# Kernel optimization log

Measured on AMD Instinct MI355X. Metric: run time of the kernel, lower is better.

Reference implementation:

```python
import jax, jax.numpy as jnp
import numpy as np
from jax import lax

P = 16        # patch_size
F = 4         # fourier_freq
E = 8         # num_experts
G = 8         # groupnorm groups = min(8, out_channel)
CIN = 128
COUT = 128
EPS = 1e-5


def conv2d(x, w):
    # x: [B,C,H,W], w: [O,I,kh,kw], stride 1, SAME padding
    return lax.conv_general_dilated(x, w, (1, 1), 'SAME',
                                    dimension_numbers=('NCHW', 'OIHW', 'NCHW'))


def group_norm(x, g, b):
    B, C, H, W = x.shape
    xg = x.reshape(B, G, C // G, H, W)
    m = xg.mean(axis=(2, 3, 4), keepdims=True)
    v = xg.var(axis=(2, 3, 4), keepdims=True)
    xn = ((xg - m) * lax.rsqrt(v + EPS)).reshape(B, C, H, W)
    return xn * g[None, :, None, None] + b[None, :, None, None]


def silu(x):
    return x * jax.nn.sigmoid(x)


def fourier_feats(Hp, Wp):
    # Fourier positional encoding of patch centers -> [Hp, Wp, 4F] (= gate_channel)
    cy = (jnp.arange(Hp, dtype=jnp.float32) + 0.5) / Hp
    cx = (jnp.arange(Wp, dtype=jnp.float32) + 0.5) / Wp
    freqs = (2.0 ** jnp.arange(F, dtype=jnp.float32)) * jnp.pi
    ay = cy[:, None] * freqs[None, :]            # [Hp, F]
    ax = cx[:, None] * freqs[None, :]            # [Wp, F]
    fy = jnp.concatenate([jnp.sin(ay), jnp.cos(ay)], axis=-1)  # [Hp, 2F]
    fx = jnp.concatenate([jnp.sin(ax), jnp.cos(ax)], axis=-1)  # [Wp, 2F]
    return jnp.concatenate([
        jnp.broadcast_to(fy[:, None, :], (Hp, Wp, 2 * F)),
        jnp.broadcast_to(fx[None, :, :], (Hp, Wp, 2 * F)),
    ], axis=-1)


def setup_inputs() -> dict:
    key = jax.random.key(0)
    ks = jax.random.split(key, 5)
    B, H, W = 8, 128, 128
    x = jax.random.normal(ks[0], (B, CIN, H, W), dtype=jnp.float32)
    expert_w = jax.random.normal(ks[1], (E, COUT, CIN, 3, 3), dtype=jnp.float32) * 0.02
    expert_g = jnp.ones((E, COUT), dtype=jnp.float32)
    expert_b = jnp.zeros((E, COUT), dtype=jnp.float32)
    router_w = jax.random.normal(ks[2], (4 * F, E), dtype=jnp.float32) * 0.1
    router_b = jnp.zeros((E,), dtype=jnp.float32)
    merge_g = jnp.ones((COUT,), dtype=jnp.float32)
    merge_b = jnp.zeros((COUT,), dtype=jnp.float32)
    gamma = jnp.ones((1,), dtype=jnp.float32) * 0.01
    post_w = jax.random.normal(ks[3], (COUT, COUT, 3, 3), dtype=jnp.float32) * 0.02
    post_g = jnp.ones((COUT,), dtype=jnp.float32)
    post_b = jnp.zeros((COUT,), dtype=jnp.float32)
    return {'x': x, 'expert_w': expert_w, 'expert_g': expert_g, 'expert_b': expert_b,
            'router_w': router_w, 'router_b': router_b, 'merge_g': merge_g,
            'merge_b': merge_b, 'gamma': gamma, 'post_w': post_w,
            'post_g': post_g, 'post_b': post_b}


def reference(x, expert_w, expert_g, expert_b, router_w, router_b,
              merge_g, merge_b, gamma, post_w, post_g, post_b):
    B, C, H, W = x.shape
    Hp, Wp = H // P, W // P

    # RouterGate: positional Fourier features -> per-patch expert weights
    feats = fourier_feats(Hp, Wp)                       # [Hp, Wp, 4F]
    logits = feats @ router_w + router_b                # [Hp, Wp, E]
    wts = jax.nn.softmax(logits, axis=-1)               # [Hp, Wp, E]

    # ConvExperts: conv3x3 -> GN -> SiLU + residual, vmapped over experts
    def expert(w, g, b):
        return silu(group_norm(conv2d(x, w), g, b)) + x

    outs = jax.vmap(expert)(expert_w, expert_g, expert_b)  # [E, B, C, H, W]

    # Broadcast patch weights to pixel resolution and merge
    wmap = jnp.repeat(jnp.repeat(wts, P, axis=0), P, axis=1)  # [H, W, E]
    merged = jnp.einsum('ebchw,hwe->bchw', outs, wmap)        # [B, C, H, W]

    # merge GN + SiLU, gamma-scaled residual
    y = x + gamma[0] * silu(group_norm(merged, merge_g, merge_b))

    # post block: conv3x3 (no bias) -> GN -> SiLU
    out = silu(group_norm(conv2d(y, post_w), post_g, post_b))
    return out
```

## Files before the change

### kernel.cpp

```cpp
#include <hip/hip_runtime.h>
#include <hip/hip_bf16.h>


typedef __attribute__((ext_vector_type(8))) short bf16x8;
typedef __attribute__((ext_vector_type(4))) float f32x4;
typedef __attribute__((ext_vector_type(2))) float f32x2;
typedef __attribute__((ext_vector_type(8))) unsigned short u16x8;
typedef __attribute__((ext_vector_type(4))) unsigned short u16x4;
typedef __attribute__((ext_vector_type(2))) unsigned int u32x2;
typedef __attribute__((ext_vector_type(2))) int i32x2;
typedef __attribute__((ext_vector_type(2))) long lx2;

__device__ __forceinline__ float b2f(unsigned short u) {
  unsigned int v = ((unsigned int)u) << 16;
  return __builtin_bit_cast(float, v);
}
__device__ __forceinline__ unsigned short f2b(float f) {
  __hip_bfloat16 h = __float2bfloat16(f);
  return __builtin_bit_cast(unsigned short, h);
}
__device__ __forceinline__ float fsilu(float x) {
  float e = __expf(-x);
  return x * __builtin_amdgcn_rcpf(1.f + e);
}
__device__ __forceinline__ void gll16(const void* g, void* l) {
  __builtin_amdgcn_global_load_lds(
      (const __attribute__((address_space(1))) unsigned int*)g,
      (__attribute__((address_space(3))) unsigned int*)l, 16, 0, 0);
}
__device__ __forceinline__ unsigned char f2fp8(float v) {
  return (unsigned char)(__builtin_amdgcn_cvt_pk_fp8_f32(v, v, 0, false) & 0xff);
}

#define PLANE8 8652800ull

__global__ void k_router(const float* __restrict__ rw, const float* __restrict__ rb,
                         float* __restrict__ wts) {
  int t = threadIdx.x;
  if (t >= 64) return;
  int py = t >> 3, px = t & 7;
  float cy = (py + 0.5f) / 8.f, cx = (px + 0.5f) / 8.f;
  const float PI = 3.14159265358979323846f;
  float f[16];
#pragma unroll
  for (int k = 0; k < 4; ++k) {
    float fr = (float)(1 << k) * PI;
    f[k] = sinf(cy * fr); f[4 + k] = cosf(cy * fr);
    f[8 + k] = sinf(cx * fr); f[12 + k] = cosf(cx * fr);
  }
  float lg[8], mx = -1e30f;
#pragma unroll
  for (int e = 0; e < 8; ++e) {
    float a = rb[e];
#pragma unroll
    for (int k = 0; k < 16; ++k) a += f[k] * rw[k * 8 + e];
    lg[e] = a; mx = fmaxf(mx, a);
  }
  float s = 0.f;
#pragma unroll
  for (int e = 0; e < 8; ++e) { lg[e] = __expf(lg[e] - mx); s += lg[e]; }
  float inv = 1.f / s;
#pragma unroll
  for (int e = 0; e < 8; ++e) wts[t * 8 + e] = lg[e] * inv;
}

__global__ void k_zborder(unsigned short* __restrict__ xpu,
                          unsigned char* __restrict__ xp8) {
  int idx = blockIdx.x * 256 + threadIdx.x;
  if (idx >= 8 * 516) return;
  int b = idx / 516, pxi = idx - b * 516;
  int r, c;
  if (pxi < 130)      { r = 0;   c = pxi; }
  else if (pxi < 260) { r = 129; c = pxi - 130; }
  else if (pxi < 388) { r = pxi - 260 + 1; c = 0; }
  else                { r = pxi - 388 + 1; c = 129; }
  size_t pix = (size_t)(b * 130 + r) * 130 + c;
  unsigned short* p = xpu + pix * 128;
#pragma unroll
  for (int j = 0; j < 16; ++j) *(u16x8*)(p + j * 8) = (u16x8)0;
#pragma unroll
  for (int cc = 0; cc < 2; ++cc) {
    f32x4* q = (f32x4*)(xp8 + cc * PLANE8 + pix * 64);
#pragma unroll
    for (int j = 0; j < 4; ++j) q[j] = (f32x4)0.f;
  }
}

__global__ void k_build_xpad(const float* __restrict__ x, __hip_bfloat16* __restrict__ xp,
                             unsigned char* __restrict__ xp8) {
  int bx = blockIdx.x;
  int wb = bx & 1, cib = (bx >> 1) & 1;
  int h = (bx >> 2) & 127, b = bx >> 9;
  int w0 = wb * 64, ci0 = cib * 64;
  __shared__ float t[64][65];
  int tid = threadIdx.x;
#pragma unroll
  for (int r = 0; r < 16; ++r) {
    int idx = r * 256 + tid;
    int i = idx >> 6, j = idx & 63;
    t[i][j] = x[(((size_t)b * 128 + ci0 + i) * 128 + h) * 128 + w0 + j];
  }
  __syncthreads();
  unsigned short* xpu = (unsigned short*)xp;
#pragma unroll
  for (int r = 0; r < 2; ++r) {
    int s = r * 256 + tid;
    int px = s >> 3, cg = s & 7;
    size_t pixbase = ((size_t)b * 130 + h + 1) * 130 + (w0 + px + 1);
    float v[8];
    u16x8 bv;
#pragma unroll
    for (int k = 0; k < 8; ++k) { v[k] = t[cg * 8 + k][px]; bv[k] = f2b(v[k]); }
    int ci = ci0 + cg * 8;
    *(u16x8*)(xpu + pixbase * 128 + ci) = bv;
    int pl = ci >> 6, cl = ci & 63;
    int kg = (cl >> 3) & 3, c = cl >> 5;
    int pk0 = __builtin_amdgcn_cvt_pk_fp8_f32(v[0], v[1], 0, false);
    pk0 = __builtin_amdgcn_cvt_pk_fp8_f32(v[2], v[3], pk0, true);
    int pk1 = __builtin_amdgcn_cvt_pk_fp8_f32(v[4], v[5], 0, false);
    pk1 = __builtin_amdgcn_cvt_pk_fp8_f32(v[6], v[7], pk1, true);
    i32x2 pk = {pk0, pk1};
    *(i32x2*)(xp8 + (size_t)pl * PLANE8 + pixbase * 64 + kg * 16 + c * 8) = pk;
  }
}

__global__ void k_build_w(const float* __restrict__ src, __hip_bfloat16* __restrict__ dst) {
  int o = blockIdx.x * 256 + threadIdx.x;
  if (o >= 147456) return;
  int cl = o & 31, co = (o >> 5) & 127;
  int r9 = o >> 12;
  int tp = r9 % 9, cc = r9 / 9;
  int ci = cc * 32 + cl;
  ((unsigned short*)dst)[o] = f2b(src[((size_t)co * 128 + ci) * 9 + tp]);
}

__global__ void k_build_w8(const float* __restrict__ src, unsigned char* __restrict__ dst) {
  int o = blockIdx.x * 256 + threadIdx.x;
  if (o >= 1179648) return;
  int e = o / 147456;
  int r = o - e * 147456;
  int cc2 = r / 73728;
  int r2 = r - cc2 * 73728;
  int tp = r2 >> 13;
  int r3 = r2 & 8191;
  int co = r3 >> 6, p = r3 & 63;
  int kg = p >> 4, c = (p >> 3) & 1, j = p & 7;
  int ci = cc2 * 64 + c * 32 + kg * 8 + j;
  dst[o] = f2fp8(src[(((size_t)e * 128 + co) * 128 + ci) * 9 + tp]);
}

template <int G>
__global__ __launch_bounds__(512, 2) void k_conv8(
    const unsigned char* __restrict__ xp8, const unsigned char* __restrict__ wt8,
    unsigned char* __restrict__ out8base, float* __restrict__ partials) {
  __shared__ __align__(16) char smem[90112];
  const int cpx = (G * 512) >> 3;
  const int nid = (blockIdx.x & 7) * cpx + (blockIdx.x >> 3);
  const int eg = nid & (G - 1);
  const int t0 = nid / G;
  const int b = t0 >> 6, rp = t0 & 63, h0 = rp * 2;
  const unsigned char* wt = wt8 + (size_t)eg * 147456;
  unsigned char* out8 = out8base + (size_t)eg * 16777216ull;

  const int tid = threadIdx.x;
  const int lane = tid & 63, wid = tid >> 6;
  const int wm = wid >> 1, wn = wid & 1;
  const int rl = lane & 15, kg = lane >> 4;
  const int rowA = wm >> 1;
  const int colA = (wm & 1) * 64;

  int aoff[3][4], boff[3][4];
#pragma unroll
  for (int mb = 0; mb < 4; ++mb) {
    int col = colA + mb * 16 + rl;
#pragma unroll
    for (int kx = 0; kx < 3; ++kx) {
      int px = col + kx;
      aoff[kx][mb] = (rowA * 160 + px) * 64 + (kg ^ ((px >> 1) & 3)) * 16;
    }
  }
#pragma unroll
  for (int kx = 0; kx < 3; ++kx)
#pragma unroll
    for (int nb = 0; nb < 4; ++nb) {
      int co = wn * 64 + nb * 16 + rl;
      boff[kx][nb] = 20480 + ((kx * 128 + co) * 4 + (kg ^ ((co >> 1) & 3))) * 16;
    }

  int soff[6], loff[6];
  bool isA[6];
#pragma unroll
  for (int it = 0; it < 6; ++it) {
    int s = it * 512 + tid;
    if (s < 1280) {
      int rw = (s >= 640) ? 1 : 0;
      int off = s - rw * 640;
      int px = off >> 2, q = off & 3;
      int qg = q ^ ((px >> 1) & 3);
      isA[it] = true;
      soff[it] = rw * 8320 + px * 64 + qg * 16;
    } else {
      int s2 = s - 1280;
      int tap = s2 >> 9, r3 = s2 & 511;
      int co = r3 >> 2, q = r3 & 3;
      int qg = q ^ ((co >> 1) & 3);
      isA[it] = false;
      soff[it] = tap * 8192 + co * 64 + qg * 16;
    }
    loff[it] = s * 16;
  }

  f32x4 acc[4][4] = {};

#define STG8(bi, u)                                                            \
  {                                                                            \
    const int cc2_ = (u) / 3, ky_ = (u) % 3;                                   \
    char* D = smem + (bi) * 45056;                                             \
    const unsigned char* abase =                                               \
        xp8 + (size_t)cc2_ * PLANE8 + (size_t)(b * 130 + h0 + ky_) * 8320;     \
    const unsigned char* bbase = wt + cc2_ * 73728 + ky_ * 24576;              \
    _Pragma("unroll")                                                          \
    for (int it = 0; it < 5; ++it)                                             \
      gll16((isA[it] ? abase : bbase) + soff[it], D + loff[it]);               \
    if (tid < 256) gll16(bbase + soff[5], D + loff[5]);                        \
  }

  STG8(0, 0);
  for (int u = 0; u < 6; ++u) {
    const int cur = u & 1;
    __syncthreads();
    if (u + 1 < 6) STG8(cur ^ 1, u + 1);
    const char* Al = smem + cur * 45056;
#pragma unroll
    for (int kx = 0; kx < 3; ++kx) {
      lx2 av[4], bv[4];
#pragma unroll
      for (int mb = 0; mb < 4; ++mb) av[mb] = *(const lx2*)(Al + aoff[kx][mb]);
#pragma unroll
      for (int nb = 0; nb < 4; ++nb) bv[nb] = *(const lx2*)(Al + boff[kx][nb]);
#pragma unroll
      for (int c = 0; c < 2; ++c)
#pragma unroll
        for (int mb = 0; mb < 4; ++mb)
#pragma unroll
          for (int nb = 0; nb < 4; ++nb)
            acc[mb][nb] = __builtin_amdgcn_mfma_f32_16x16x32_fp8_fp8(
                bv[nb][c], av[mb][c], acc[mb][nb], 0, 0, 0);
    }
  }
#undef STG8

  float sv[4] = {0, 0, 0, 0}, qv[4] = {0, 0, 0, 0};
#pragma unroll
  for (int mb = 0; mb < 4; ++mb) {
    int px = colA + mb * 16 + rl;
    int h = h0 + rowA, w = px;
    size_t base = (((size_t)b * 128 + h) * 128 + w) * 128;
#pragma unroll
    for (int nb = 0; nb < 4; ++nb) {
      int co0 = wn * 64 + nb * 16 + kg * 4;
      f32x4 v = acc[mb][nb];
#pragma unroll
      for (int j = 0; j < 4; ++j) { sv[nb] += v[j]; qv[nb] += v[j] * v[j]; }
      int pk = __builtin_amdgcn_cvt_pk_fp8_f32(v[0], v[1], 0, false);
      pk = __builtin_amdgcn_cvt_pk_fp8_f32(v[2], v[3], pk, true);
      *(int*)(out8 + base + co0) = pk;
    }
  }
  __syncthreads();
  float* sg = (float*)smem;
  if (tid < 16) sg[tid] = 0.f;
  __syncthreads();
#pragma unroll
  for (int nb = 0; nb < 4; ++nb) {
    float a = sv[nb], q = qv[nb];
#pragma unroll
    for (int o = 32; o > 0; o >>= 1) { a += __shfl_down(a, o); q += __shfl_down(q, o); }
    if (lane == 0) {
      int g = wn * 4 + nb;
      atomicAdd(&sg[g * 2 + 0], a);
      atomicAdd(&sg[g * 2 + 1], q);
    }
  }
  __syncthreads();
  if (tid < 16)
    partials[((size_t)(eg * 8 + b) * 64 + rp) * 16 + tid] = sg[tid];
}

__global__ __launch_bounds__(256, 2) void k_conv(
    const unsigned short* __restrict__ xpu, const unsigned short* __restrict__ wtu,
    unsigned short* __restrict__ outu, float* __restrict__ partials) {
  __shared__ __align__(16) char smem[69632];
  const int bx0 = blockIdx.x;
  const int nid = (bx0 & 7) * 128 + (bx0 >> 3);
  const int b = nid >> 7, h0 = nid & 127;
  const int tid = threadIdx.x;
  const int lane = tid & 63, wid = tid >> 6;
  const int wm = wid >> 1, wn = wid & 1;
  const int rl = lane & 15, kg = lane >> 4;

  int aoff[3][4], boff[3][4];
#pragma unroll
  for (int mb = 0; mb < 4; ++mb) {
    int w = wm * 64 + mb * 16 + rl;
#pragma unroll
    for (int kx = 0; kx < 3; ++kx) {
      int px = w + kx;
      aoff[kx][mb] = (px * 4 + (kg ^ ((px >> 1) & 3))) * 16;
    }
  }
#pragma unroll
  for (int kx = 0; kx < 3; ++kx)
#pragma unroll
    for (int nb = 0; nb < 4; ++nb) {
      int co = wn * 64 + nb * 16 + rl;
      boff[kx][nb] = 10240 + ((kx * 128 + co) * 4 + (kg ^ ((co >> 1) & 3))) * 16;
    }

  int asoff[3], aloff[3];
#pragma unroll
  for (int it = 0; it < 3; ++it) {
    int s = it * 256 + tid;
    int px = s >> 2, q = s & 3;
    int qg = q ^ ((px >> 1) & 3);
    asoff[it] = px * 256 + (q ^ ((px >> 1) & 3)) * 16;
    (void)qg;
    aloff[it] = s * 16;
  }
  int bsoff[6], bloff[6];
#pragma unroll
  for (int jt = 0; jt < 6; ++jt) {
    int s2 = jt * 256 + tid;
    int t3 = s2 >> 9;
    int r3 = s2 & 511;
    int co = r3 >> 2, q = r3 & 3;
    int qg = q ^ ((co >> 1) & 3);
    bsoff[jt] = t3 * 8192 + co * 64 + qg * 16;
    bloff[jt] = 10240 + s2 * 16;
  }

  f32x4 acc[4][4] = {};
  const char* xpb = (const char*)xpu;
  const char* wtb = (const char*)wtu;

#define STAGE(bi, u)                                                          \
  {                                                                           \
    const int cc_ = (u) / 3, ky_ = (u) % 3;                                   \
    char* D = smem + (bi) * 34816;                                            \
    const char* abase = xpb + (size_t)(b * 130 + h0 + ky_) * 33280 + cc_ * 64;\
    const char* bbase = wtb + cc_ * 73728 + ky_ * 24576;                      \
    _Pragma("unroll")                                                         \
    for (int it = 0; it < 2; ++it)                                            \
      gll16(abase + asoff[it], D + aloff[it]);                                \
    if (tid < 128) gll16(abase + asoff[2], D + aloff[2]);                     \
    _Pragma("unroll")                                                         \
    for (int jt = 0; jt < 6; ++jt)                                            \
      gll16(bbase + bsoff[jt], D + bloff[jt]);                                \
  }

  STAGE(0, 0);
  for (int u = 0; u < 12; ++u) {
    const int cur = u & 1;
    __syncthreads();
    if (u + 1 < 12) STAGE(cur ^ 1, u + 1);
    char* Al = smem + cur * 34816;
#pragma unroll
    for (int kx = 0; kx < 3; ++kx) {
      bf16x8 aF[4], bF[4];
#pragma unroll
      for (int mb = 0; mb < 4; ++mb) aF[mb] = *(const bf16x8*)(Al + aoff[kx][mb]);
#pragma unroll
      for (int nb = 0; nb < 4; ++nb) bF[nb] = *(const bf16x8*)(Al + boff[kx][nb]);
#pragma unroll
      for (int mb = 0; mb < 4; ++mb)
#pragma unroll
        for (int nb = 0; nb < 4; ++nb)
          acc[mb][nb] = __builtin_amdgcn_mfma_f32_16x16x32_bf16(
              bF[nb], aF[mb], acc[mb][nb], 0, 0, 0);
    }
  }
#undef STAGE

  float sv[4] = {0, 0, 0, 0}, qv[4] = {0, 0, 0, 0};
#pragma unroll
  for (int mb = 0; mb < 4; ++mb) {
    int w = wm * 64 + mb * 16 + rl;
    size_t base = (((size_t)b * 128 + h0) * 128 + w) * 128;
#pragma unroll
    for (int nb = 0; nb < 4; ++nb) {
      int co0 = wn * 64 + nb * 16 + kg * 4;
      u16x4 pk;
#pragma unroll
      for (int j = 0; j < 4; ++j) {
        float v = acc[mb][nb][j];
        pk[j] = f2b(v);
        sv[nb] += v; qv[nb] += v * v;
      }
      *(u16x4*)(outu + base + co0) = pk;
    }
  }
  __syncthreads();
  float* sg = (float*)smem;
  if (tid < 16) sg[tid] = 0.f;
  __syncthreads();
#pragma unroll
  for (int nb = 0; nb < 4; ++nb) {
    float a = sv[nb], q = qv[nb];
#pragma unroll
    for (int o = 32; o > 0; o >>= 1) { a += __shfl_down(a, o); q += __shfl_down(q, o); }
    if (lane == 0) {
      int g = wn * 4 + nb;
      atomicAdd(&sg[g * 2 + 0], a);
      atomicAdd(&sg[g * 2 + 1], q);
    }
  }
  __syncthreads();
  if (tid < 16) partials[(size_t)nid * 16 + tid] = sg[tid];
}

__global__ void k_redstats(const float* __restrict__ partials, float* __restrict__ stats,
                           int nper) {
  int set = blockIdx.x;
  const float* p = partials + (size_t)set * 8 * nper * 16;
  float* st = stats + set * 128;
  int t = threadIdx.x;
  int o = t >> 2, j = t & 3;
  int b = o >> 4, slot = o & 15;
  int chunk = nper >> 2;
  float s = 0.f;
  for (int i = j * chunk; i < (j + 1) * chunk; ++i)
    s += p[((size_t)b * nper + i) * 16 + slot];
  s += __shfl_xor(s, 1);
  s += __shfl_xor(s, 2);
  if (j == 0) st[o] = s;
}

__global__ void k_redstats2(const float* __restrict__ p2, float* __restrict__ st) {
  int o = blockIdx.x;
  int b = o >> 4, slot = o & 15;
  float s = 0.f;
  for (int i = threadIdx.x; i < 1024; i += 256)
    s += p2[((size_t)b * 1024 + i) * 16 + slot];
#pragma unroll
  for (int off = 32; off > 0; off >>= 1) s += __shfl_down(s, off);
  __shared__ float wsm[4];
  int lane = threadIdx.x & 63, wv = threadIdx.x >> 6;
  if (lane == 0) wsm[wv] = s;
  __syncthreads();
  if (threadIdx.x == 0) st[o] = wsm[0] + wsm[1] + wsm[2] + wsm[3];
}

template <int NEXP>
__global__ void k_merge(const unsigned char* __restrict__ c0,
                        const unsigned char* __restrict__ c1,
                        const unsigned char* __restrict__ c2,
                        const unsigned char* __restrict__ c3,
                        const float* __restrict__ st, const float* __restrict__ eg,
                        const float* __restrict__ eb, const float* __restrict__ wts,
                        unsigned short* __restrict__ merged,
                        const unsigned short* __restrict__ xp,
                        float* __restrict__ partials2, int e0, int flags) {
  __shared__ float sg[16];
  int tid = threadIdx.x;
  if (tid < 16) sg[tid] = 0.f;
  __syncthreads();
  size_t idx = ((size_t)blockIdx.x * 256 + tid) * 8;
  int co0 = (int)(idx & 127);
  size_t pix = idx >> 7;
  int w = (int)(pix & 127), h = (int)((pix >> 7) & 127), b = (int)(pix >> 14);
  int g = co0 >> 4;
  const float cnt = 16.f * 128.f * 128.f;
  int patch = (h >> 4) * 8 + (w >> 4);
  const unsigned char* cs[4] = {c0, c1, c2, c3};
  float a[8] = {0, 0, 0, 0, 0, 0, 0, 0};
#pragma unroll
  for (int k = 0; k < NEXP; ++k) {
    int e = e0 + k;
    float mean = st[e * 128 + (b * 8 + g) * 2] / cnt;
    float var = st[e * 128 + (b * 8 + g) * 2 + 1] / cnt - mean * mean;
    float rstd = rsqrtf(var + 1e-5f);
    float we = wts[patch * 8 + e];
    f32x4 g0 = *(const f32x4*)(eg + e * 128 + co0);
    f32x4 g1 = *(const f32x4*)(eg + e * 128 + co0 + 4);
    f32x4 b0 = *(const f32x4*)(eb + e * 128 + co0);
    f32x4 b1 = *(const f32x4*)(eb + e * 128 + co0 + 4);
    u32x2 cv = *(const u32x2*)(cs[k] + idx);
    f32x2 d0 = __builtin_amdgcn_cvt_pk_f32_fp8(cv[0], false);
    f32x2 d1 = __builtin_amdgcn_cvt_pk_f32_fp8(cv[0], true);
    f32x2 d2 = __builtin_amdgcn_cvt_pk_f32_fp8(cv[1], false);
    f32x2 d3 = __builtin_amdgcn_cvt_pk_f32_fp8(cv[1], true);
    float d[8] = {d0[0], d0[1], d1[0], d1[1], d2[0], d2[1], d3[0], d3[1]};
#pragma unroll
    for (int i = 0; i < 8; ++i) {
      float gi = (i < 4) ? g0[i] : g1[i - 4];
      float bi = (i < 4) ? b0[i] : b1[i - 4];
      float A = rstd * gi;
      float B = bi - mean * A;
      a[i] += we * fsilu(d[i] * A + B);
    }
  }
  if (flags & 1) {
    u16x8 mv = *(const u16x8*)(merged + idx);
#pragma unroll
    for (int i = 0; i < 8; ++i) a[i] += b2f(mv[i]);
  }
  u16x8 out;
  float s = 0.f, q = 0.f;
  if (flags & 2) {
    const unsigned short* xr =
        xp + (((size_t)b * 130 + h + 1) * 130 + (w + 1)) * 128 + co0;
    u16x8 xv = *(const u16x8*)xr;
#pragma unroll
    for (int i = 0; i < 8; ++i) {
      a[i] += b2f(xv[i]);
      out[i] = f2b(a[i]);
      float rv = b2f(out[i]);
      s += rv; q += rv * rv;
    }
  } else {
#pragma unroll
    for (int i = 0; i < 8; ++i) out[i] = f2b(a[i]);
  }
  *(u16x8*)(merged + idx) = out;
  if (flags & 2) {
    atomicAdd(&sg[g * 2 + 0], s);
    atomicAdd(&sg[g * 2 + 1], q);
    __syncthreads();
    if (tid < 16) partials2[(size_t)blockIdx.x * 16 + tid] = sg[tid];
  }
}

__global__ void k_ypass(const unsigned short* __restrict__ merged,
                        unsigned short* __restrict__ xp,
                        const float* __restrict__ st, const float* __restrict__ mg,
                        const float* __restrict__ mbv, const float* __restrict__ gptr) {
  size_t idx = ((size_t)blockIdx.x * 256 + threadIdx.x) * 8;
  int co0 = (int)(idx & 127);
  size_t pix = idx >> 7;
  int w = (int)(pix & 127), h = (int)((pix >> 7) & 127), b = (int)(pix >> 14);
  int g = co0 >> 4;
  const float cnt = 16.f * 128.f * 128.f;
  float mean = st[(b * 8 + g) * 2] / cnt;
  float var = st[(b * 8 + g) * 2 + 1] / cnt - mean * mean;
  float rstd = rsqrtf(var + 1e-5f);
  float gm = gptr[0];
  unsigned short* xr = xp + (((size_t)b * 130 + h + 1) * 130 + (w + 1)) * 128 + co0;
  u16x8 xv = *(const u16x8*)xr;
  u16x8 mv = *(const u16x8*)(merged + idx);
  u16x8 yv;
#pragma unroll
  for (int i = 0; i < 8; ++i) {
    float xf = b2f(xv[i]);
    float M = b2f(mv[i]);
    float xn = (M - mean) * rstd * mg[co0 + i] + mbv[co0 + i];
    yv[i] = f2b(xf + gm * fsilu(xn));
  }
  *(u16x8*)xr = yv;
}

__global__ void k_final(const __hip_bfloat16* __restrict__ conv, const float* __restrict__ st,
                        const float* __restrict__ pg, const float* __restrict__ pb,
                        float* __restrict__ out) {
  int bx = blockIdx.x;
  int wb = bx & 1, h = (bx >> 1) & 127, b = bx >> 8;
  int w0 = wb * 64;
  __shared__ float t[64][129];
  int tid = threadIdx.x;
  const float cnt = 16.f * 128.f * 128.f;
  const unsigned short* cu = (const unsigned short*)conv;
#pragma unroll
  for (int r = 0; r < 32; ++r) {
    int e2 = r * 256 + tid;
    int co = e2 & 127, wl = e2 >> 7;
    int g = co >> 4;
    float mean = st[(b * 8 + g) * 2] / cnt;
    float var = st[(b * 8 + g) * 2 + 1] / cnt - mean * mean;
    float rstd = rsqrtf(var + 1e-5f);
    float v = b2f(cu[(((size_t)b * 128 + h) * 128 + w0 + wl) * 128 + co]);
    float xn = (v - mean) * rstd * pg[co] + pb[co];
    t[wl][co] = fsilu(xn);
  }
  __syncthreads();
#pragma unroll
  for (int r = 0; r < 8; ++r) {
    int f = r * 256 + tid;
    int jb = f & 15, co = f >> 4;
    f32x4 o;
#pragma unroll
    for (int j = 0; j < 4; ++j) o[j] = t[jb * 4 + j][co];
    *(f32x4*)&out[(((size_t)b * 128 + co) * 128 + h) * 128 + w0 + jb * 4] = o;
  }
}

extern "C" void kernel_launch(void* const* d_in, const int* in_sizes, int n_in,
                              void* d_out, int out_size, void* d_ws, size_t ws_size,
                              hipStream_t stream) {
  const float* x        = (const float*)d_in[0];
  const float* expert_w = (const float*)d_in[1];
  const float* expert_g = (const float*)d_in[2];
  const float* expert_b = (const float*)d_in[3];
  const float* router_w = (const float*)d_in[4];
  const float* router_b = (const float*)d_in[5];
  const float* merge_g  = (const float*)d_in[6];
  const float* merge_b  = (const float*)d_in[7];
  const float* gamma    = (const float*)d_in[8];
  const float* post_w   = (const float*)d_in[9];
  const float* post_g   = (const float*)d_in[10];
  const float* post_b   = (const float*)d_in[11];

  char* ws = (char*)d_ws;
  float* wts            = (float*)(ws + 0);
  float* stats          = (float*)(ws + 2048);
  float* partials       = (float*)(ws + 8192);
  float* partials2      = (float*)(ws + 270336);
  unsigned short* wtbp  = (unsigned short*)(ws + 794624);
  unsigned char* wtb8   = (unsigned char*)(ws + 1089536);
  unsigned short* xpad  = (unsigned short*)(ws + 2269184);
  unsigned char* xpad8  = (unsigned char*)(ws + 36888576);
  const size_t BUFS = 54198272ull;
  const size_t FB = 16777216ull;
  const size_t NEED2 = BUFS + 2 * FB + 33554432ull;
  const size_t NEED4 = BUFS + 4 * FB + 33554432ull;
  int nbuf = (ws_size >= NEED4) ? 4 : 2;
  unsigned char* bufs0 = (unsigned char*)(ws + BUFS);
  unsigned short* merged = (unsigned short*)(ws + BUFS + (size_t)nbuf * FB);
  unsigned short* pbuf = (unsigned short*)(ws + BUFS);
  if (ws_size < NEED2) {
    hipMemsetAsync(d_out, 0, (size_t)out_size * 4, stream);
    return;
  }

  k_zborder<<<17, 256, 0, stream>>>(xpad, xpad8);
  k_router<<<1, 64, 0, stream>>>(router_w, router_b, wts);
  k_build_xpad<<<4096, 256, 0, stream>>>(x, (__hip_bfloat16*)xpad, xpad8);
  k_build_w<<<576, 256, 0, stream>>>(post_w, (__hip_bfloat16*)wtbp);
  k_build_w8<<<4608, 256, 0, stream>>>(expert_w, wtb8);

  if (nbuf == 4) {
    for (int p = 0; p < 2; ++p) {
      k_conv8<4><<<2048, 512, 0, stream>>>(xpad8, wtb8 + (size_t)(p * 4) * 147456,
                                           bufs0, partials);
      k_redstats<<<4, 512, 0, stream>>>(partials, stats + p * 4 * 128, 64);
      int flags = (p > 0 ? 1 : 0) | (p == 1 ? 2 : 0);
      k_merge<4><<<8192, 256, 0, stream>>>(bufs0, bufs0 + FB, bufs0 + 2 * FB,
                                           bufs0 + 3 * FB, stats, expert_g, expert_b,
                                           wts, merged, xpad, partials2, p * 4, flags);
    }
  } else {
    for (int p = 0; p < 4; ++p) {
      k_conv8<2><<<1024, 512, 0, stream>>>(xpad8, wtb8 + (size_t)(p * 2) * 147456,
                                           bufs0, partials);
      k_redstats<<<2, 512, 0, stream>>>(partials, stats + p * 2 * 128, 64);
      int flags = (p > 0 ? 1 : 0) | (p == 3 ? 2 : 0);
      k_merge<2><<<8192, 256, 0, stream>>>(bufs0, bufs0 + FB, bufs0, bufs0 + FB,
                                           stats, expert_g, expert_b, wts, merged,
                                           xpad, partials2, p * 2, flags);
    }
  }
  k_redstats2<<<128, 256, 0, stream>>>(partials2, stats + 8 * 128);
  k_ypass<<<8192, 256, 0, stream>>>(merged, xpad, stats + 8 * 128, merge_g, merge_b, gamma);
  k_conv<<<1024, 256, 0, stream>>>(xpad, wtbp, pbuf, partials);
  k_redstats<<<1, 512, 0, stream>>>(partials, stats + 9 * 128, 128);
  k_final<<<2048, 256, 0, stream>>>((const __hip_bfloat16*)pbuf, stats + 9 * 128,
                                    post_g, post_b, (float*)d_out);
}
```

Before: 434.0 us.

## Shrink fp8 expert conv tile to one row with per-tap B staging

The fp8 expert convolution moves from 512-thread blocks covering two output rows to 256-thread blocks covering one row. Weight tiles are now staged one tap at a time with their own double buffer, separate from the input row buffer. This cuts shared memory from about 90KB to 36KB so more blocks can be resident per CU. The cost is that weight tiles are reused across fewer pixels, there are more barriers (18 stages instead of 6), and the stats partials double in count.

```diff
diff --git a/kernel.cpp b/kernel.cpp
--- a/kernel.cpp
+++ b/kernel.cpp
@@ -150,15 +150,15 @@
 }
 
 template <int G>
-__global__ __launch_bounds__(512, 2) void k_conv8(
+__global__ __launch_bounds__(256, 4) void k_conv8(
     const unsigned char* __restrict__ xp8, const unsigned char* __restrict__ wt8,
     unsigned char* __restrict__ out8base, float* __restrict__ partials) {
-  __shared__ __align__(16) char smem[90112];
-  const int cpx = (G * 512) >> 3;
+  __shared__ __align__(16) char smem[36864];
+  const int cpx = G * 128;
   const int nid = (blockIdx.x & 7) * cpx + (blockIdx.x >> 3);
   const int eg = nid & (G - 1);
   const int t0 = nid / G;
-  const int b = t0 >> 6, rp = t0 & 63, h0 = rp * 2;
+  const int b = t0 >> 7, h0 = t0 & 127;
   const unsigned char* wt = wt8 + (size_t)eg * 147456;
   unsigned char* out8 = out8base + (size_t)eg * 16777216ull;
 
@@ -166,96 +166,85 @@
   const int lane = tid & 63, wid = tid >> 6;
   const int wm = wid >> 1, wn = wid & 1;
   const int rl = lane & 15, kg = lane >> 4;
-  const int rowA = wm >> 1;
-  const int colA = (wm & 1) * 64;
-
-  int aoff[3][4], boff[3][4];
+
+  int aoff[3][4];
+  int boff[4];
 #pragma unroll
   for (int mb = 0; mb < 4; ++mb) {
-    int col = colA + mb * 16 + rl;
+    int col = wm * 64 + mb * 16 + rl;
 #pragma unroll
     for (int kx = 0; kx < 3; ++kx) {
       int px = col + kx;
-      aoff[kx][mb] = (rowA * 160 + px) * 64 + (kg ^ ((px >> 1) & 3)) * 16;
-    }
-  }
-#pragma unroll
-  for (int kx = 0; kx < 3; ++kx)
-#pragma unroll
-    for (int nb = 0; nb < 4; ++nb) {
-      int co = wn * 64 + nb * 16 + rl;
-      boff[kx][nb] = 20480 + ((kx * 128 + co) * 4 + (kg ^ ((co >> 1) & 3))) * 16;
-    }
-
-  int soff[6], loff[6];
-  bool isA[6];
-#pragma unroll
-  for (int it = 0; it < 6; ++it) {
-    int s = it * 512 + tid;
-    if (s < 1280) {
-      int rw = (s >= 640) ? 1 : 0;
-      int off = s - rw * 640;
-      int px = off >> 2, q = off & 3;
-      int qg = q ^ ((px >> 1) & 3);
-      isA[it] = true;
-      soff[it] = rw * 8320 + px * 64 + qg * 16;
-    } else {
-      int s2 = s - 1280;
-      int tap = s2 >> 9, r3 = s2 & 511;
-      int co = r3 >> 2, q = r3 & 3;
-      int qg = q ^ ((co >> 1) & 3);
-      isA[it] = false;
-      soff[it] = tap * 8192 + co * 64 + qg * 16;
-    }
-    loff[it] = s * 16;
-  }
+      aoff[kx][mb] = px * 64 + (kg ^ ((px >> 1) & 3)) * 16;
+    }
+  }
+#pragma unroll
+  for (int nb = 0; nb < 4; ++nb) {
+    int co = wn * 64 + nb * 16 + rl;
+    boff[nb] = (co * 4 + (kg ^ ((co >> 1) & 3))) * 16;
+  }
+
+  const int stg = (tid >> 2) * 64 + ((tid & 3) ^ ((tid >> 3) & 3)) * 16;
+  const int ldso = tid * 16;
 
   f32x4 acc[4][4] = {};
 
-#define STG8(bi, u)                                                            \
+#define STGA(ab, cc2_, ky_)                                                    \
   {                                                                            \
-    const int cc2_ = (u) / 3, ky_ = (u) % 3;                                   \
-    char* D = smem + (bi) * 45056;                                             \
     const unsigned char* abase =                                               \
-        xp8 + (size_t)cc2_ * PLANE8 + (size_t)(b * 130 + h0 + ky_) * 8320;     \
-    const unsigned char* bbase = wt + cc2_ * 73728 + ky_ * 24576;              \
-    _Pragma("unroll")                                                          \
-    for (int it = 0; it < 5; ++it)                                             \
-      gll16((isA[it] ? abase : bbase) + soff[it], D + loff[it]);               \
-    if (tid < 256) gll16(bbase + soff[5], D + loff[5]);                        \
-  }
-
-  STG8(0, 0);
-  for (int u = 0; u < 6; ++u) {
-    const int cur = u & 1;
+        xp8 + (size_t)(cc2_)*PLANE8 + (size_t)(b * 130 + h0 + (ky_)) * 8320;   \
+    char* D = smem + (ab)*10240;                                               \
+    gll16(abase + stg, D + ldso);                                              \
+    gll16(abase + stg + 4096, D + ldso + 4096);                                \
+    if (tid < 128) gll16(abase + stg + 8192, D + ldso + 8192);                 \
+  }
+#define STGB(bb, cc2_, tap_)                                                   \
+  {                                                                            \
+    const unsigned char* bbase = wt + (cc2_)*73728 + (tap_)*8192;              \
+    char* D = smem + 20480 + (bb)*8192;                                        \
+    gll16(bbase + stg, D + ldso);                                              \
+    gll16(bbase + stg + 4096, D + ldso + 4096);                                \
+  }
+
+  STGA(0, 0, 0);
+  STGB(0, 0, 0);
+#pragma unroll
+  for (int u = 0; u < 18; ++u) {
     __syncthreads();
-    if (u + 1 < 6) STG8(cur ^ 1, u + 1);
-    const char* Al = smem + cur * 45056;
-#pragma unroll
-    for (int kx = 0; kx < 3; ++kx) {
-      lx2 av[4], bv[4];
-#pragma unroll
-      for (int mb = 0; mb < 4; ++mb) av[mb] = *(const lx2*)(Al + aoff[kx][mb]);
-#pragma unroll
-      for (int nb = 0; nb < 4; ++nb) bv[nb] = *(const lx2*)(Al + boff[kx][nb]);
-#pragma unroll
-      for (int c = 0; c < 2; ++c)
-#pragma unroll
-        for (int mb = 0; mb < 4; ++mb)
-#pragma unroll
-          for (int nb = 0; nb < 4; ++nb)
-            acc[mb][nb] = __builtin_amdgcn_mfma_f32_16x16x32_fp8_fp8(
-                bv[nb][c], av[mb][c], acc[mb][nb], 0, 0, 0);
-    }
-  }
-#undef STG8
+    if (u + 1 < 18) {
+      const int un = u + 1;
+      const int cc2n = un / 9, rn = un % 9;
+      STGB(un & 1, cc2n, rn);
+      if (un % 3 == 0) {
+        const int a3 = un / 3;
+        STGA(a3 & 1, a3 / 3, a3 % 3);
+      }
+    }
+    const int a3 = u / 3, kx = u % 3;
+    const char* Al = smem + (a3 & 1) * 10240;
+    const char* Bl = smem + 20480 + (u & 1) * 8192;
+    lx2 av[4], bv[4];
+#pragma unroll
+    for (int mb = 0; mb < 4; ++mb) av[mb] = *(const lx2*)(Al + aoff[kx][mb]);
+#pragma unroll
+    for (int nb = 0; nb < 4; ++nb) bv[nb] = *(const lx2*)(Bl + boff[nb]);
+#pragma unroll
+    for (int c = 0; c < 2; ++c)
+#pragma unroll
+      for (int mb = 0; mb < 4; ++mb)
+#pragma unroll
+        for (int nb = 0; nb < 4; ++nb)
+          acc[mb][nb] = __builtin_amdgcn_mfma_f32_16x16x32_fp8_fp8(
+              bv[nb][c], av[mb][c], acc[mb][nb], 0, 0, 0);
+  }
+#undef STGA
+#undef STGB
 
   float sv[4] = {0, 0, 0, 0}, qv[4] = {0, 0, 0, 0};
 #pragma unroll
   for (int mb = 0; mb < 4; ++mb) {
-    int px = colA + mb * 16 + rl;
-    int h = h0 + rowA, w = px;
-    size_t base = (((size_t)b * 128 + h) * 128 + w) * 128;
+    int px = wm * 64 + mb * 16 + rl;
+    size_t base = (((size_t)b * 128 + h0) * 128 + px) * 128;
 #pragma unroll
     for (int nb = 0; nb < 4; ++nb) {
       int co0 = wn * 64 + nb * 16 + kg * 4;
@@ -284,7 +273,7 @@
   }
   __syncthreads();
   if (tid < 16)
-    partials[((size_t)(eg * 8 + b) * 64 + rp) * 16 + tid] = sg[tid];
+    partials[(((size_t)(eg * 8 + b)) * 128 + h0) * 16 + tid] = sg[tid];
 }
 
 __global__ __launch_bounds__(256, 2) void k_conv(
@@ -322,9 +311,7 @@
   for (int it = 0; it < 3; ++it) {
     int s = it * 256 + tid;
     int px = s >> 2, q = s & 3;
-    int qg = q ^ ((px >> 1) & 3);
     asoff[it] = px * 256 + (q ^ ((px >> 1) & 3)) * 16;
-    (void)qg;
     aloff[it] = s * 16;
   }
   int bsoff[6], bloff[6];
@@ -638,9 +625,9 @@
 
   if (nbuf == 4) {
     for (int p = 0; p < 2; ++p) {
-      k_conv8<4><<<2048, 512, 0, stream>>>(xpad8, wtb8 + (size_t)(p * 4) * 147456,
+      k_conv8<4><<<4096, 256, 0, stream>>>(xpad8, wtb8 + (size_t)(p * 4) * 147456,
                                            bufs0, partials);
-      k_redstats<<<4, 512, 0, stream>>>(partials, stats + p * 4 * 128, 64);
+      k_redstats<<<4, 512, 0, stream>>>(partials, stats + p * 4 * 128, 128);
       int flags = (p > 0 ? 1 : 0) | (p == 1 ? 2 : 0);
       k_merge<4><<<8192, 256, 0, stream>>>(bufs0, bufs0 + FB, bufs0 + 2 * FB,
                                            bufs0 + 3 * FB, stats, expert_g, expert_b,
@@ -648,9 +635,9 @@
     }
   } else {
     for (int p = 0; p < 4; ++p) {
-      k_conv8<2><<<1024, 512, 0, stream>>>(xpad8, wtb8 + (size_t)(p * 2) * 147456,
+      k_conv8<2><<<2048, 256, 0, stream>>>(xpad8, wtb8 + (size_t)(p * 2) * 147456,
                                            bufs0, partials);
-      k_redstats<<<2, 512, 0, stream>>>(partials, stats + p * 2 * 128, 64);
+      k_redstats<<<2, 512, 0, stream>>>(partials, stats + p * 2 * 128, 128);
       int flags = (p > 0 ? 1 : 0) | (p == 3 ? 2 : 0);
       k_merge<2><<<8192, 256, 0, stream>>>(bufs0, bufs0 + FB, bufs0, bufs0 + FB,
                                            stats, expert_g, expert_b, wts, merged,
```

New measurement: 461.8 us. +6.4%, slower.

## Retile post conv to two rows per 512-thread block and raise MFMA priority

Applied to the files above, without the earlier changes.

The post-block bf16 conv kernel now processes two output rows per block with 512 threads (8 waves), so each staged weight tile is reused across twice as many pixels and the launch count halves. The staging offsets are unified into a single A/B loop like the fp8 expert conv, and the partial-stats count passed to the reduction drops to 64. Both conv kernels also raise wave priority around the MFMA loop so compute is favoured over the prefetch loads, and per-thread LDS offsets are computed inline to save registers. The larger LDS footprint (88KB) and bigger blocks may reduce occupancy.

```diff
diff --git a/kernel.cpp b/kernel.cpp
--- a/kernel.cpp
+++ b/kernel.cpp
@@ -187,7 +187,7 @@
       boff[kx][nb] = 20480 + ((kx * 128 + co) * 4 + (kg ^ ((co >> 1) & 3))) * 16;
     }
 
-  int soff[6], loff[6];
+  int soff[6];
   bool isA[6];
 #pragma unroll
   for (int it = 0; it < 6; ++it) {
@@ -207,7 +207,6 @@
       isA[it] = false;
       soff[it] = tap * 8192 + co * 64 + qg * 16;
     }
-    loff[it] = s * 16;
   }
 
   f32x4 acc[4][4] = {};
@@ -221,8 +220,8 @@
     const unsigned char* bbase = wt + cc2_ * 73728 + ky_ * 24576;              \
     _Pragma("unroll")                                                          \
     for (int it = 0; it < 5; ++it)                                             \
-      gll16((isA[it] ? abase : bbase) + soff[it], D + loff[it]);               \
-    if (tid < 256) gll16(bbase + soff[5], D + loff[5]);                        \
+      gll16((isA[it] ? abase : bbase) + soff[it], D + (it * 512 + tid) * 16);  \
+    if (tid < 256) gll16(bbase + soff[5], D + (5 * 512 + tid) * 16);           \
   }
 
   STG8(0, 0);
@@ -231,6 +230,7 @@
     __syncthreads();
     if (u + 1 < 6) STG8(cur ^ 1, u + 1);
     const char* Al = smem + cur * 45056;
+    __builtin_amdgcn_s_setprio(1);
 #pragma unroll
     for (int kx = 0; kx < 3; ++kx) {
       lx2 av[4], bv[4];
@@ -247,6 +247,7 @@
             acc[mb][nb] = __builtin_amdgcn_mfma_f32_16x16x32_fp8_fp8(
                 bv[nb][c], av[mb][c], acc[mb][nb], 0, 0, 0);
     }
+    __builtin_amdgcn_s_setprio(0);
   }
 #undef STG8
 
@@ -287,26 +288,27 @@
     partials[((size_t)(eg * 8 + b) * 64 + rp) * 16 + tid] = sg[tid];
 }
 
-__global__ __launch_bounds__(256, 2) void k_conv(
+__global__ __launch_bounds__(512, 2) void k_conv(
     const unsigned short* __restrict__ xpu, const unsigned short* __restrict__ wtu,
     unsigned short* __restrict__ outu, float* __restrict__ partials) {
-  __shared__ __align__(16) char smem[69632];
-  const int bx0 = blockIdx.x;
-  const int nid = (bx0 & 7) * 128 + (bx0 >> 3);
-  const int b = nid >> 7, h0 = nid & 127;
+  __shared__ __align__(16) char smem[90112];
+  const int nid = (blockIdx.x & 7) * 64 + (blockIdx.x >> 3);
+  const int b = nid >> 6, rp = nid & 63, h0 = rp * 2;
   const int tid = threadIdx.x;
   const int lane = tid & 63, wid = tid >> 6;
   const int wm = wid >> 1, wn = wid & 1;
   const int rl = lane & 15, kg = lane >> 4;
+  const int rowA = wm >> 1;
+  const int colA = (wm & 1) * 64;
 
   int aoff[3][4], boff[3][4];
 #pragma unroll
   for (int mb = 0; mb < 4; ++mb) {
-    int w = wm * 64 + mb * 16 + rl;
+    int col = colA + mb * 16 + rl;
 #pragma unroll
     for (int kx = 0; kx < 3; ++kx) {
-      int px = w + kx;
-      aoff[kx][mb] = (px * 4 + (kg ^ ((px >> 1) & 3))) * 16;
+      int px = col + kx;
+      aoff[kx][mb] = (rowA * 160 + px) * 64 + (kg ^ ((px >> 1) & 3)) * 16;
     }
   }
 #pragma unroll
@@ -314,48 +316,46 @@
 #pragma unroll
     for (int nb = 0; nb < 4; ++nb) {
       int co = wn * 64 + nb * 16 + rl;
-      boff[kx][nb] = 10240 + ((kx * 128 + co) * 4 + (kg ^ ((co >> 1) & 3))) * 16;
-    }
-
-  int asoff[3], aloff[3];
-#pragma unroll
-  for (int it = 0; it < 3; ++it) {
-    int s = it * 256 + tid;
-    int px = s >> 2, q = s & 3;
-    int qg = q ^ ((px >> 1) & 3);
-    asoff[it] = px * 256 + (q ^ ((px >> 1) & 3)) * 16;
-    (void)qg;
-    aloff[it] = s * 16;
-  }
-  int bsoff[6], bloff[6];
-#pragma unroll
-  for (int jt = 0; jt < 6; ++jt) {
-    int s2 = jt * 256 + tid;
-    int t3 = s2 >> 9;
-    int r3 = s2 & 511;
-    int co = r3 >> 2, q = r3 & 3;
-    int qg = q ^ ((co >> 1) & 3);
-    bsoff[jt] = t3 * 8192 + co * 64 + qg * 16;
-    bloff[jt] = 10240 + s2 * 16;
+      boff[kx][nb] = 20480 + ((kx * 128 + co) * 4 + (kg ^ ((co >> 1) & 3))) * 16;
+    }
+
+  int soff[6];
+  bool isA[6];
+#pragma unroll
+  for (int it = 0; it < 6; ++it) {
+    int s = it * 512 + tid;
+    if (s < 1280) {
+      int rw = (s >= 640) ? 1 : 0;
+      int off = s - rw * 640;
+      int px = off >> 2, q = off & 3;
+      int qg = q ^ ((px >> 1) & 3);
+      isA[it] = true;
+      soff[it] = rw * 33280 + px * 256 + qg * 16;
+    } else {
+      int s2 = s - 1280;
+      int tap = s2 >> 9, r3 = s2 & 511;
+      int co = r3 >> 2, q = r3 & 3;
+      int qg = q ^ ((co >> 1) & 3);
+      isA[it] = false;
+      soff[it] = tap * 8192 + co * 64 + qg * 16;
+    }
   }
 
   f32x4 acc[4][4] = {};
   const char* xpb = (const char*)xpu;
   const char* wtb = (const char*)wtu;
 
-#define STAGE(bi, u)                                                          \
-  {                                                                           \
-    const int cc_ = (u) / 3, ky_ = (u) % 3;                                   \
-    char* D = smem + (bi) * 34816;                                            \
-    const char* abase = xpb + (size_t)(b * 130 + h0 + ky_) * 33280 + cc_ * 64;\
-    const char* bbase = wtb + cc_ * 73728 + ky_ * 24576;                      \
-    _Pragma("unroll")                                                         \
-    for (int it = 0; it < 2; ++it)                                            \
-      gll16(abase + asoff[it], D + aloff[it]);                                \
-    if (tid < 128) gll16(abase + asoff[2], D + aloff[2]);                     \
-    _Pragma("unroll")                                                         \
-    for (int jt = 0; jt < 6; ++jt)                                            \
-      gll16(bbase + bsoff[jt], D + bloff[jt]);                                \
+#define STAGE(bi, u)                                                           \
+  {                                                                            \
+    const int cc_ = (u) / 3, ky_ = (u) % 3;                                    \
+    char* D = smem + (bi) * 45056;                                             \
+    const char* abase =                                                        \
+        xpb + (size_t)(b * 130 + h0 + ky_) * 33280 + cc_ * 64;                 \
+    const char* bbase = wtb + cc_ * 73728 + ky_ * 24576;                       \
+    _Pragma("unroll")                                                          \
+    for (int it = 0; it < 5; ++it)                                             \
+      gll16((isA[it] ? abase : bbase) + soff[it], D + (it * 512 + tid) * 16);  \
+    if (tid < 256) gll16(bbase + soff[5], D + (5 * 512 + tid) * 16);           \
   }
 
   STAGE(0, 0);
@@ -363,7 +363,8 @@
     const int cur = u & 1;
     __syncthreads();
     if (u + 1 < 12) STAGE(cur ^ 1, u + 1);
-    char* Al = smem + cur * 34816;
+    const char* Al = smem + cur * 45056;
+    __builtin_amdgcn_s_setprio(1);
 #pragma unroll
     for (int kx = 0; kx < 3; ++kx) {
       bf16x8 aF[4], bF[4];
@@ -378,14 +379,16 @@
           acc[mb][nb] = __builtin_amdgcn_mfma_f32_16x16x32_bf16(
               bF[nb], aF[mb], acc[mb][nb], 0, 0, 0);
     }
+    __builtin_amdgcn_s_setprio(0);
   }
 #undef STAGE
 
   float sv[4] = {0, 0, 0, 0}, qv[4] = {0, 0, 0, 0};
 #pragma unroll
   for (int mb = 0; mb < 4; ++mb) {
-    int w = wm * 64 + mb * 16 + rl;
-    size_t base = (((size_t)b * 128 + h0) * 128 + w) * 128;
+    int px = colA + mb * 16 + rl;
+    int h = h0 + rowA;
+    size_t base = (((size_t)b * 128 + h) * 128 + px) * 128;
 #pragma unroll
     for (int nb = 0; nb < 4; ++nb) {
       int co0 = wn * 64 + nb * 16 + kg * 4;
@@ -659,8 +662,8 @@
   }
   k_redstats2<<<128, 256, 0, stream>>>(partials2, stats + 8 * 128);
   k_ypass<<<8192, 256, 0, stream>>>(merged, xpad, stats + 8 * 128, merge_g, merge_b, gamma);
-  k_conv<<<1024, 256, 0, stream>>>(xpad, wtbp, pbuf, partials);
-  k_redstats<<<1, 512, 0, stream>>>(partials, stats + 9 * 128, 128);
+  k_conv<<<512, 512, 0, stream>>>(xpad, wtbp, pbuf, partials);
+  k_redstats<<<1, 512, 0, stream>>>(partials, stats + 9 * 128, 64);
   k_final<<<2048, 256, 0, stream>>>((const __hip_bfloat16*)pbuf, stats + 9 * 128,
                                     post_g, post_b, (float*)d_out);
 }
```

New measurement: 448.3 us. +3.3%, slower.
